# Optimization experiments

Measured on AMD Instinct MI355X. Metric: run time of the kernel, lower is better.

Reference implementation:

```python
import jax, jax.numpy as jnp
import numpy as np
import math

N, D, H, KV, DH, E, F_, CH = 2048, 1024, 16, 4, 64, 8, 2048, 64
VOCAB = 32000
EPS = 1e-6
THETA = 10000.0
DT = 0.1
BASE_SCALE = 10.0


def rmsnorm(x, w):
    var = jnp.mean(jnp.square(x), axis=-1, keepdims=True)
    return x * jax.lax.rsqrt(var + EPS) * w


def rope_tables(positions):
    inv_freq = THETA ** (-jnp.arange(0, DH, 2, dtype=jnp.float32) / DH)  # [DH/2]
    ang = positions.astype(jnp.float32)[:, None] * inv_freq              # [N, DH/2]
    return jnp.cos(ang), jnp.sin(ang)


def apply_rotary(x, cos, sin):
    # x: [N, heads, DH]; NeoX half-split rotation
    x1, x2 = jnp.split(x, 2, axis=-1)
    c, s = cos[:, None, :], sin[:, None, :]
    return jnp.concatenate([x1 * c - x2 * s, x2 * c + x1 * s], axis=-1)


def setup_inputs() -> dict:
    key = jax.random.key(0)
    ks = jax.random.split(key, 20)
    nrm = lambda k, shp, std: (jax.random.normal(k, shp) * std).astype(jnp.float32)
    inp = {
        'hidden': jax.random.normal(ks[0], (N, D), jnp.float32),
        'positions': jnp.arange(N, dtype=jnp.int32),
        'velocity': jax.random.normal(ks[1], (N, D), jnp.float32) * 0.1,
        'token_ids': jax.random.randint(ks[2], (N,), 0, VOCAB),
        'mu_prev': jax.random.normal(ks[3], (N, D), jnp.float32) * 0.1,
        'ln1_w': jnp.ones((D,), jnp.float32),
        'ln2_w': jnp.ones((D,), jnp.float32),
        'wq': nrm(ks[4], (D, H * DH), 0.02),
        'wk': nrm(ks[5], (D, KV * DH), 0.02),
        'wv': nrm(ks[6], (D, KV * DH), 0.02),
        'wo': nrm(ks[7], (H * DH, D), 0.02),
        'w_mu_q': nrm(ks[8], (D, H * DH), 0.01),
        'w_mu_k': nrm(ks[9], (D, KV * DH), 0.01),
        'w_mu_v': nrm(ks[10], (D, KV * DH), 0.01),
        'qnorm_w': jnp.ones((DH,), jnp.float32),
        'knorm_w': jnp.ones((DH,), jnp.float32),
        'dyn_mu': jnp.zeros((D,), jnp.float32),
        'dyn_mu_proj_w': nrm(ks[11], (D, D), 0.01),
        'ctrl_in_w': nrm(ks[12], (2 * D, CH), 0.02),
        'ctrl_in_b': jnp.zeros((CH,), jnp.float32),
        'ctrl_out_w': nrm(ks[13], (CH, 3 * D), 0.01),
        'ctrl_out_b': jnp.concatenate([jnp.full((D,), 2.2), jnp.full((D,), -2.2), jnp.zeros((D,))]).astype(jnp.float32),
        'mu_router_w': nrm(ks[14], (D, E), 0.01),
        'w_gate': nrm(ks[15], (E, D, F_), 0.02),
        'w_up': nrm(ks[16], (E, D, F_), 0.02),
        'w_down': nrm(ks[17], (E, F_, D), 0.02),
    }
    return inp


def reference(hidden, positions, velocity, token_ids, mu_prev,
              ln1_w, ln2_w, wq, wk, wv, wo, w_mu_q, w_mu_k, w_mu_v,
              qnorm_w, knorm_w, dyn_mu, dyn_mu_proj_w,
              ctrl_in_w, ctrl_in_b, ctrl_out_w, ctrl_out_b,
              mu_router_w, w_gate, w_up, w_down):
    residual = hidden
    h = rmsnorm(hidden, ln1_w)
    # --- mu-guided GQA attention ---
    q = (h @ wq + mu_prev @ w_mu_q).reshape(N, H, DH)
    k = (h @ wk + mu_prev @ w_mu_k).reshape(N, KV, DH)
    v = (h @ wv + mu_prev @ w_mu_v).reshape(N, KV, DH)
    q = rmsnorm(q, qnorm_w)
    k = rmsnorm(k, knorm_w)
    cos, sin = rope_tables(positions)
    q = apply_rotary(q, cos, sin)
    k = apply_rotary(k, cos, sin)
    groups = H // KV
    k = jnp.repeat(k, groups, axis=1)  # [N, H, DH]
    v = jnp.repeat(v, groups, axis=1)
    scale = 1.0 / math.sqrt(DH)
    scores = jnp.einsum('nhd,mhd->hnm', q, k) * scale
    attn = jax.nn.softmax(scores, axis=-1)
    o = jnp.einsum('hnm,mhd->nhd', attn, v).reshape(N, H * DH) @ wo
    # --- INL dynamics (PID) ---
    hv = jnp.concatenate([o, velocity], axis=-1)
    ctrl = jax.nn.silu(hv @ ctrl_in_w + ctrl_in_b)
    co = ctrl @ ctrl_out_w + ctrl_out_b
    alpha_raw, beta_raw, gate_raw = co[:, :D], co[:, D:2 * D], co[:, 2 * D:]
    alpha = jax.nn.sigmoid(alpha_raw)
    beta = jnp.minimum(jax.nn.softplus(beta_raw), 2.0)
    gate = jax.nn.sigmoid(gate_raw)
    mu_cur = dyn_mu + o @ dyn_mu_proj_w
    err = o - mu_cur
    v_next = jnp.clip(alpha * velocity - beta * err, -10.0, 10.0)
    h_next = o + DT * gate * v_next
    hidden = residual + h_next
    # --- mu-guided token-routed MoE MLP ---
    residual2 = hidden
    x = rmsnorm(hidden, ln2_w)
    base_ids = (token_ids % E).astype(jnp.int32)
    mu_logits = mu_cur @ mu_router_w                        # [N, E]
    combined = jax.nn.one_hot(base_ids, E) * BASE_SCALE + mu_logits
    expert_ids = jnp.argmax(combined, axis=-1)              # [N]
    g = jnp.einsum('nd,edf->enf', x, w_gate)                # [E, N, F]
    u = jnp.einsum('nd,edf->enf', x, w_up)
    mid = jax.nn.silu(g) * u
    y_all = jnp.einsum('enf,efd->end', mid, w_down)         # [E, N, D]
    sel = jax.nn.one_hot(expert_ids, E)                     # [N, E]
    y = jnp.einsum('ne,end->nd', sel, y_all)
    hidden = residual2 + y
    return (hidden, v_next, mu_cur)
```

## Files before the change

### kernel.cpp

```cpp
#include <hip/hip_runtime.h>
#include <hip/hip_bf16.h>
#include <math.h>

typedef __hip_bfloat16 bf16;
typedef __attribute__((ext_vector_type(8))) short short8;
typedef __attribute__((ext_vector_type(4))) short short4v;
typedef __attribute__((ext_vector_type(4))) float floatx4;

#define N_TOK 2048
#define DM    1024
#define NH    16
#define NKV   4
#define DH    64
#define NE    8
#define FF    2048
#define CH    64
#define QSCL  0.18033688011112042f

__device__ __forceinline__ float b2f(bf16 x) { return __bfloat162float(x); }
__device__ __forceinline__ bf16  f2b(float x) { return __float2bfloat16(x); }
__device__ __forceinline__ short f2s(float x) { bf16 t = __float2bfloat16(x); return *(short*)&t; }

#define MFMA16(a, b, c) __builtin_amdgcn_mfma_f32_16x16x32_bf16(a, b, c, 0, 0, 0)

#define GLL16(g, l) __builtin_amdgcn_global_load_lds( \
    (const __attribute__((address_space(1))) void*)(g), \
    (__attribute__((address_space(3))) void*)(l), 16, 0, 0)

__device__ __forceinline__ float blockReduceSum256(float v) {
    __shared__ float tmp[4];
    #pragma unroll
    for (int m = 1; m < 64; m <<= 1) v += __shfl_xor(v, m, 64);
    if ((threadIdx.x & 63) == 0) tmp[threadIdx.x >> 6] = v;
    __syncthreads();
    float r = tmp[0] + tmp[1] + tmp[2] + tmp[3];
    __syncthreads();
    return r;
}

struct TEnt {
    const float* src; bf16* dst;
    long sstride, dstride;
    int sN, ldk, tN, tilesPer, start;
};
struct TTab { TEnt t[13]; };

template <int TK>
__global__ __launch_bounds__(256) void k_transpose_all(TTab tab, int base,
                                                       int* counts, int* fill) {
    if (base == 0 && blockIdx.x == 0 && threadIdx.x < NE) {
        counts[threadIdx.x] = 0;
        fill[threadIdx.x] = 0;
    }
    int b = blockIdx.x + base;
    int wi = 0;
    #pragma unroll
    for (int i = 1; i < 13; i++) if (b >= tab.t[i].start) wi = i;
    const TEnt& w = tab.t[wi];
    int local = b - w.start;
    int e = local / w.tilesPer; local -= e * w.tilesPer;
    int kt = local / w.tN, nt = local - kt * w.tN;
    const float* s = w.src + (long)e * w.sstride + (long)(kt * TK) * w.sN + nt * 64;
    bf16* d = w.dst + (long)e * w.dstride + (long)(nt * 64) * w.ldk + kt * TK;

    __shared__ short t16[64 * TK];
    int tid = threadIdx.x;
    int c4 = (tid & 15) * 4;

    #pragma unroll
    for (int j = 0; j < (TK / 8 + 15) / 16; j++) {
        int kk8 = 8 * ((tid >> 4) + 16 * j);
        if (kk8 < TK) {
            float4 rr[8];
            #pragma unroll
            for (int t = 0; t < 8; t++)
                rr[t] = *(const float4*)(s + (long)(kk8 + t) * w.sN + c4);
            #pragma unroll
            for (int q = 0; q < 4; q++) {
                int n = c4 + q;
                int ks = kk8 ^ ((n & 7) << 3);
                short8 o;
                #pragma unroll
                for (int t = 0; t < 8; t++) o[t] = f2s(((const float*)&rr[t])[q]);
                *(short8*)&t16[n * TK + ks] = o;
            }
        }
    }
    __syncthreads();
    const int cpr = TK / 8;
    #pragma unroll
    for (int rnd = 0; rnd < TK / 32; rnd++) {
        int id = tid + rnd * 256;
        int n = id / cpr;
        int kc = (id % cpr) * 8;
        int ks = kc ^ ((n & 7) << 3);
        short8 o = *(const short8*)&t16[n * TK + ks];
        *(short8*)(d + (long)n * w.ldk + kc) = o;
    }
}

__global__ __launch_bounds__(256) void k_prep(
    const float* __restrict__ hidden, const float* __restrict__ ln1_w,
    const float* __restrict__ mu_prev, const float* __restrict__ velocity,
    bf16* __restrict__ catA, bf16* __restrict__ ctrlA)
{
    int n = blockIdx.x, tid = threadIdx.x;
    float ss = 0.f, vals[4];
    #pragma unroll
    for (int i = 0; i < 4; i++) {
        int c = tid + i * 256;
        vals[i] = hidden[(long)n * DM + c];
        ss += vals[i] * vals[i];
        catA[(long)n * 2048 + 1024 + c] = f2b(mu_prev[(long)n * DM + c]);
        ctrlA[(long)n * 2048 + 1024 + c] = f2b(velocity[(long)n * DM + c]);
    }
    float tot = blockReduceSum256(ss);
    float r = rsqrtf(tot / (float)DM + 1e-6f);
    #pragma unroll
    for (int i = 0; i < 4; i++) {
        int c = tid + i * 256;
        catA[(long)n * 2048 + c] = f2b(vals[i] * r * ln1_w[c]);
    }
}

#define GEMM_WRITE  1
#define GEMM_BIAS   2
#define GEMM_WRITEB 4
#define GEMM_DOWN   8

__global__ __launch_bounds__(256) void k_gemm(
    const bf16* __restrict__ A, int lda,
    const bf16* __restrict__ Bt, int ldb, long strideBe,
    float* __restrict__ C, int ldc,
    const float* __restrict__ bias,
    bf16* __restrict__ Cb, int ldcb,
    int K, int flags,
    int nsplit, long strideKc,
    const int* __restrict__ grp_cnt,
    const int* __restrict__ perm,
    float* __restrict__ outp)
{
    __shared__ __align__(16) short As[128 * 32];
    __shared__ __align__(16) short Bs[128 * 32];
    int tid = threadIdx.x;
    int e = blockIdx.z, kc = 0;
    if (nsplit > 1) { e = blockIdx.z / nsplit; kc = blockIdx.z % nsplit; }
    int rowBase, rowsValid;
    const bf16* Bp = Bt;
    if (grp_cnt) {
        int r0 = 0;
        #pragma unroll
        for (int i = 0; i < NE; i++) r0 += (i < e) ? grp_cnt[i] : 0;
        int r1 = r0 + grp_cnt[e];
        int rt = blockIdx.y * 128;
        rowsValid = (r1 - r0) - rt;
        if (rowsValid <= 0) return;
        if (rowsValid > 128) rowsValid = 128;
        rowBase = r0 + rt;
        Bp = Bt + (long)e * strideBe;
    } else {
        rowBase = blockIdx.y * 128;
        rowsValid = 128;
    }
    int n0 = blockIdx.x * 128;
    int Kc = K / nsplit;
    int kbeg = kc * Kc, kend = kbeg + Kc;

    floatx4 acc[4][4];
    #pragma unroll
    for (int i = 0; i < 4; i++)
        #pragma unroll
        for (int j = 0; j < 4; j++) acc[i][j] = (floatx4){0.f, 0.f, 0.f, 0.f};

    int wave = tid >> 6, lane = tid & 63;
    int wm = (wave >> 1) * 64, wn = (wave & 1) * 64;
    int lrow = lane & 15, quad = lane >> 4;

    int c0 = wave * 2;
    int srow0 = c0 * 16 + (lane >> 2);
    int srow1 = (c0 + 1) * 16 + (lane >> 2);
    int skoff = (lane & 3) * 8;
    short* ldsA0 = As + c0 * 512;
    short* ldsA1 = As + (c0 + 1) * 512;
    short* ldsB0 = Bs + c0 * 512;
    short* ldsB1 = Bs + (c0 + 1) * 512;

    for (int k0 = kbeg; k0 < kend; k0 += 32) {
        if (srow0 < rowsValid) GLL16(A + (long)(rowBase + srow0) * lda + k0 + skoff, ldsA0);
        if (srow1 < rowsValid) GLL16(A + (long)(rowBase + srow1) * lda + k0 + skoff, ldsA1);
        GLL16(Bp + (long)(n0 + srow0) * ldb + k0 + skoff, ldsB0);
        GLL16(Bp + (long)(n0 + srow1) * ldb + k0 + skoff, ldsB1);
        __syncthreads();
        short8 af[4], bfr[4];
        #pragma unroll
        for (int mi = 0; mi < 4; mi++)
            af[mi] = *(const short8*)(&As[(wm + mi * 16 + lrow) * 32 + quad * 8]);
        #pragma unroll
        for (int ni = 0; ni < 4; ni++)
            bfr[ni] = *(const short8*)(&Bs[(wn + ni * 16 + lrow) * 32 + quad * 8]);
        #pragma unroll
        for (int mi = 0; mi < 4; mi++)
            #pragma unroll
            for (int ni = 0; ni < 4; ni++)
                acc[mi][ni] = MFMA16(af[mi], bfr[ni], acc[mi][ni]);
        __syncthreads();
    }

    #pragma unroll
    for (int mi = 0; mi < 4; mi++) {
        #pragma unroll
        for (int ni = 0; ni < 4; ni++) {
            #pragma unroll
            for (int r = 0; r < 4; r++) {
                int rl = wm + mi * 16 + quad * 4 + r;
                if (rl >= rowsValid) continue;
                int grow = rowBase + rl;
                int gcol = n0 + wn + ni * 16 + lrow;
                float v = acc[mi][ni][r];
                if (nsplit > 1) {
                    C[kc * strideKc + (long)grow * ldc + gcol] = v;
                    continue;
                }
                if (flags & GEMM_BIAS) v += bias[gcol];
                if (flags & GEMM_DOWN) {
                    int tok = perm[grow];
                    float* o = &outp[(long)tok * ldc + gcol];
                    *o = *o + v;
                } else {
                    if (flags & GEMM_WRITE) C[(long)grow * ldc + gcol] = v;
                    if (flags & GEMM_WRITEB) Cb[(long)grow * ldcb + gcol] = f2b(v);
                }
            }
        }
    }
}

__global__ __launch_bounds__(256) void k_red_wo(const float* __restrict__ p,
                                                float* __restrict__ o_f,
                                                bf16* __restrict__ ctrlA) {
    int n = blockIdx.x, tid = threadIdx.x;
    #pragma unroll
    for (int i = 0; i < 4; i++) {
        int c = tid + i * 256;
        float v = p[(long)n * DM + c] + p[(long)N_TOK * DM + (long)n * DM + c];
        o_f[(long)n * DM + c] = v;
        ctrlA[(long)n * 2048 + c] = f2b(v);
    }
}

__global__ __launch_bounds__(256) void k_red_down(const float* __restrict__ p,
                                                  const int* __restrict__ perm,
                                                  float* __restrict__ out0) {
    int r = blockIdx.x, tid = threadIdx.x;
    int tok = perm[r];
    #pragma unroll
    for (int i = 0; i < 4; i++) {
        int c = tid + i * 256;
        long idx = (long)r * DM + c;
        float v = p[idx] + p[(long)N_TOK * DM + idx] +
                  p[(long)2 * N_TOK * DM + idx] + p[(long)3 * N_TOK * DM + idx];
        out0[(long)tok * DM + c] += v;
    }
}

__global__ __launch_bounds__(256) void k_ctrl_gemm(
    const bf16* __restrict__ A,
    const bf16* __restrict__ Bt,
    float* __restrict__ part)
{
    __shared__ __align__(16) short As[128 * 32];
    __shared__ __align__(16) short Bs[64 * 32];
    int tid = threadIdx.x;
    int rowBase = blockIdx.x * 128;
    int kbeg = blockIdx.y * 256;
    int wave = tid >> 6, lane = tid & 63;
    int wm = wave * 32, lrow = lane & 15, quad = lane >> 4;
    int srow = lane >> 2, skoff = (lane & 3) * 8;

    floatx4 acc[2][4];
    #pragma unroll
    for (int i = 0; i < 2; i++)
        #pragma unroll
        for (int j = 0; j < 4; j++) acc[i][j] = (floatx4){0.f, 0.f, 0.f, 0.f};

    short* ldsA0 = As + (wave * 2) * 512;
    short* ldsA1 = As + (wave * 2 + 1) * 512;
    short* ldsB  = Bs + wave * 512;

    for (int k0 = kbeg; k0 < kbeg + 256; k0 += 32) {
        GLL16(A + (long)(rowBase + wave * 32 + srow) * 2048 + k0 + skoff, ldsA0);
        GLL16(A + (long)(rowBase + wave * 32 + 16 + srow) * 2048 + k0 + skoff, ldsA1);
        GLL16(Bt + (long)(wave * 16 + srow) * 2048 + k0 + skoff, ldsB);
        __syncthreads();
        short8 af[2], bfr[4];
        af[0] = *(const short8*)(&As[(wm + lrow) * 32 + quad * 8]);
        af[1] = *(const short8*)(&As[(wm + 16 + lrow) * 32 + quad * 8]);
        #pragma unroll
        for (int ni = 0; ni < 4; ni++)
            bfr[ni] = *(const short8*)(&Bs[(ni * 16 + lrow) * 32 + quad * 8]);
        #pragma unroll
        for (int mi = 0; mi < 2; mi++)
            #pragma unroll
            for (int ni = 0; ni < 4; ni++)
                acc[mi][ni] = MFMA16(af[mi], bfr[ni], acc[mi][ni]);
        __syncthreads();
    }
    #pragma unroll
    for (int mi = 0; mi < 2; mi++)
        #pragma unroll
        for (int ni = 0; ni < 4; ni++)
            #pragma unroll
            for (int r = 0; r < 4; r++) {
                int grow = rowBase + wm + mi * 16 + quad * 4 + r;
                part[((long)blockIdx.y * N_TOK + grow) * 64 + ni * 16 + lrow] = acc[mi][ni][r];
            }
}

__global__ __launch_bounds__(256) void k_silu_ctrl(const float* __restrict__ part,
                                                   const float* __restrict__ b,
                                                   bf16* __restrict__ out) {
    int i4 = (blockIdx.x * 256 + threadIdx.x) * 4;
    float4 a = *(const float4*)(b + (i4 & 63));
    #pragma unroll
    for (int kc = 0; kc < 8; kc++) {
        float4 p = *(const float4*)(part + (long)kc * (N_TOK * 64) + i4);
        a.x += p.x; a.y += p.y; a.z += p.z; a.w += p.w;
    }
    short4v o;
    o[0] = f2s(a.x / (1.f + __expf(-a.x)));
    o[1] = f2s(a.y / (1.f + __expf(-a.y)));
    o[2] = f2s(a.z / (1.f + __expf(-a.z)));
    o[3] = f2s(a.w / (1.f + __expf(-a.w)));
    *(short4v*)(out + i4) = o;
}

__global__ __launch_bounds__(256) void k_qkv_post(
    const float* __restrict__ qkvp, const int* __restrict__ positions,
    const float* __restrict__ qnw, const float* __restrict__ knw,
    bf16* __restrict__ q, bf16* __restrict__ k, bf16* __restrict__ v)
{
    int n = blockIdx.x;
    int wave = threadIdx.x >> 6, lane = threadIdx.x & 63;
    float pos = (float)positions[n];
    int i = lane & 31;
    float invf = exp2f(-(float)(2 * i) * (13.287712379549449f / 64.f));
    float ang = pos * invf;
    float c = cosf(ang), s = sinf(ang);

    #pragma unroll
    for (int si = 0; si < 6; si++) {
        int slot = wave + si * 4;
        long base = (long)n * 1536 +
                    (slot < 16 ? slot * 64
                               : (slot < 20 ? 1024 + (slot - 16) * 64
                                            : 1280 + (slot - 20) * 64));
        float val = qkvp[base + lane] + qkvp[(long)N_TOK * 1536 + base + lane];
        if (slot < 20) {
            float ss = val * val;
            #pragma unroll
            for (int m = 1; m < 64; m <<= 1) ss += __shfl_xor(ss, m, 64);
            float r = rsqrtf(ss / 64.f + 1e-6f);
            float wn = (slot < 16 ? qnw[lane] : knw[lane]);
            float xn = val * r * wn;
            float partner = __shfl_xor(xn, 32, 64);
            float out = (lane < 32) ? (xn * c - partner * s) : (xn * c + partner * s);
            if (slot < 16) q[((long)n * NH + slot) * 64 + lane] = f2b(out * QSCL);
            else           k[((long)n * NKV + (slot - 16)) * 64 + lane] = f2b(out);
        } else {
            v[((long)n * NKV + (slot - 20)) * 64 + lane] = f2b(val);
        }
    }
}

__global__ __launch_bounds__(256) void k_vt(const bf16* __restrict__ v,
                                            bf16* __restrict__ vt) {
    __shared__ short tile[64][65];
    int kv = blockIdx.z, n0 = blockIdx.x * 64;
    int tid = threadIdx.x;
    int c = tid & 63, r4 = tid >> 6;
    const short* vs = (const short*)v;
    #pragma unroll
    for (int i = 0; i < 16; i++) {
        int r = i * 4 + r4;
        tile[r][c] = vs[(long)(n0 + r) * 256 + kv * 64 + c];
    }
    __syncthreads();
    #pragma unroll
    for (int i = 0; i < 16; i++) {
        int d = i * 4 + r4;
        ((short*)vt)[(long)(kv * 64 + d) * 2048 + n0 + c] = tile[c][d];
    }
}

__device__ __forceinline__ int lds_idx(int row, int col_sh) {
    int byteoff = col_sh * 2;
    byteoff ^= (row & 7) << 4;
    return row * 64 + (byteoff >> 1);
}

__global__ __launch_bounds__(256) void k_attn(
    const bf16* __restrict__ q, const bf16* __restrict__ k,
    const bf16* __restrict__ vt,
    float* __restrict__ opart, float2* __restrict__ ml)
{
    const int h = blockIdx.y;
    const int qbase = blockIdx.x * 64;
    const int z = blockIdx.z;
    const int kvh = h >> 2;
    __shared__ __align__(16) short Ks[64 * 64];
    __shared__ __align__(16) short Vt[64 * 64];
    __shared__ __align__(16) short Ps[64 * 64];
    int tid = threadIdx.x, wave = tid >> 6, lane = tid & 63;
    int lrow = lane & 15, quad = lane >> 4;

    const bf16* qp = q + ((long)(qbase + wave * 16 + lrow) * NH + h) * 64;
    short8 aq0 = *(const short8*)(qp + quad * 8);
    short8 aq1 = *(const short8*)(qp + 32 + quad * 8);

    short8 bones;
    #pragma unroll
    for (int j = 0; j < 8; j++) bones[j] = (short)0x3F80;

    const int lin0 = tid, lin1 = tid + 256;
    const int sr0 = lin0 >> 3, sc0 = (lin0 & 7) * 8;
    const int sr1 = lin1 >> 3, sc1 = (lin1 & 7) * 8;
    const int wi0 = lds_idx(sr0, sc0), wi1 = lds_idx(sr1, sc1);

    const int kt0 = z * (N_TOK / 4);
    const bf16* kg0 = k + ((long)(kt0 + sr0) * NKV + kvh) * 64 + sc0;
    const bf16* kg1 = k + ((long)(kt0 + sr1) * NKV + kvh) * 64 + sc1;
    const bf16* vg0 = vt + (long)(kvh * 64 + sr0) * 2048 + kt0 + sc0;
    const bf16* vg1 = vt + (long)(kvh * 64 + sr1) * 2048 + kt0 + sc1;

    *(short8*)&Ks[wi0] = *(const short8*)kg0;
    *(short8*)&Ks[wi1] = *(const short8*)kg1;
    *(short8*)&Vt[wi0] = *(const short8*)vg0;
    *(short8*)&Vt[wi1] = *(const short8*)vg1;

    float m_i[4];
    floatx4 lacc = (floatx4){0.f, 0.f, 0.f, 0.f};
    floatx4 oacc[4];
    #pragma unroll
    for (int r = 0; r < 4; r++) m_i[r] = -1e30f;
    #pragma unroll
    for (int di = 0; di < 4; di++) oacc[di] = (floatx4){0.f, 0.f, 0.f, 0.f};
    __syncthreads();

    const int NT = (N_TOK / 4) / 64;
    for (int t = 0; t < NT; t++) {
        bool pf = (t + 1 < NT);
        short8 nk0, nk1, nv0, nv1;
        if (pf) {
            long ko = (long)(t + 1) * (64 * NKV * 64);
            int  vo = (t + 1) * 64;
            nk0 = *(const short8*)(kg0 + ko);
            nk1 = *(const short8*)(kg1 + ko);
            nv0 = *(const short8*)(vg0 + vo);
            nv1 = *(const short8*)(vg1 + vo);
        }

        floatx4 sv[4];
        __builtin_amdgcn_s_setprio(1);
        #pragma unroll
        for (int kn = 0; kn < 4; kn++) {
            short8 b0 = *(const short8*)&Ks[lds_idx(kn * 16 + lrow, quad * 8)];
            short8 b1 = *(const short8*)&Ks[lds_idx(kn * 16 + lrow, 32 + quad * 8)];
            floatx4 tt = (floatx4){0.f, 0.f, 0.f, 0.f};
            tt = MFMA16(aq0, b0, tt);
            tt = MFMA16(aq1, b1, tt);
            sv[kn] = tt;
        }
        __builtin_amdgcn_s_setprio(0);

        float mx[4];
        #pragma unroll
        for (int r = 0; r < 4; r++) {
            float m0 = fmaxf(fmaxf(sv[0][r], sv[1][r]), fmaxf(sv[2][r], sv[3][r]));
            #pragma unroll
            for (int msk = 1; msk < 16; msk <<= 1) m0 = fmaxf(m0, __shfl_xor(m0, msk, 64));
            mx[r] = m0;
        }
        int ok = (mx[0] <= m_i[0] + 8.f) & (mx[1] <= m_i[1] + 8.f) &
                 (mx[2] <= m_i[2] + 8.f) & (mx[3] <= m_i[3] + 8.f);
        if (!__all(ok)) {
            #pragma unroll
            for (int r = 0; r < 4; r++) {
                float mn = fmaxf(m_i[r], mx[r]);
                float al = exp2f(m_i[r] - mn);
                m_i[r] = mn;
                lacc[r] *= al;
                #pragma unroll
                for (int di = 0; di < 4; di++) oacc[di][r] *= al;
            }
        }
        #pragma unroll
        for (int kn = 0; kn < 4; kn++)
            #pragma unroll
            for (int r = 0; r < 4; r++)
                sv[kn][r] = exp2f(sv[kn][r] - m_i[r]);

        #pragma unroll
        for (int kn = 0; kn < 4; kn++)
            #pragma unroll
            for (int r = 0; r < 4; r++)
                Ps[lds_idx(wave * 16 + quad * 4 + r, kn * 16 + lrow)] = f2s(sv[kn][r]);
        __syncthreads();

        short8 ap0 = *(const short8*)&Ps[lds_idx(wave * 16 + lrow, quad * 8)];
        short8 ap1 = *(const short8*)&Ps[lds_idx(wave * 16 + lrow, 32 + quad * 8)];
        __builtin_amdgcn_s_setprio(1);
        lacc = MFMA16(ap0, bones, lacc);
        lacc = MFMA16(ap1, bones, lacc);
        #pragma unroll
        for (int di = 0; di < 4; di++) {
            short8 bv0 = *(const short8*)&Vt[lds_idx(di * 16 + lrow, quad * 8)];
            short8 bv1 = *(const short8*)&Vt[lds_idx(di * 16 + lrow, 32 + quad * 8)];
            oacc[di] = MFMA16(ap0, bv0, oacc[di]);
            oacc[di] = MFMA16(ap1, bv1, oacc[di]);
        }
        __builtin_amdgcn_s_setprio(0);
        __syncthreads();

        if (pf) {
            *(short8*)&Ks[wi0] = nk0;
            *(short8*)&Ks[wi1] = nk1;
            *(short8*)&Vt[wi0] = nv0;
            *(short8*)&Vt[wi1] = nv1;
            __syncthreads();
        }
    }

    #pragma unroll
    for (int di = 0; di < 4; di++)
        #pragma unroll
        for (int r = 0; r < 4; r++) {
            int n = qbase + wave * 16 + quad * 4 + r;
            opart[((long)z * N_TOK + n) * DM + h * 64 + di * 16 + lrow] = oacc[di][r];
        }
    if (lrow == 0) {
        #pragma unroll
        for (int r = 0; r < 4; r++) {
            int n = qbase + wave * 16 + quad * 4 + r;
            ml[(long)(z * NH + h) * N_TOK + n] = make_float2(m_i[r], lacc[r]);
        }
    }
}

__global__ __launch_bounds__(256) void k_attn_merge(
    const float* __restrict__ opart, const float2* __restrict__ ml,
    bf16* __restrict__ attn_out)
{
    int n = blockIdx.x, tid = threadIdx.x;
    __shared__ float2 sml[4][NH];
    if (tid < 64) {
        int zz = tid >> 4, hh = tid & 15;
        sml[zz][hh] = ml[(long)(zz * NH + hh) * N_TOK + n];
    }
    __syncthreads();
    #pragma unroll
    for (int i = 0; i < 4; i++) {
        int c = tid + i * 256;
        int h = c >> 6;
        float M = fmaxf(fmaxf(sml[0][h].x, sml[1][h].x),
                        fmaxf(sml[2][h].x, sml[3][h].x));
        float num = 0.f, den = 0.f;
        #pragma unroll
        for (int zz = 0; zz < 4; zz++) {
            float w = exp2f(sml[zz][h].x - M);
            num += w * opart[((long)zz * N_TOK + n) * DM + c];
            den += w * sml[zz][h].y;
        }
        attn_out[(long)n * DM + c] = f2b(num / den);
    }
}

__global__ __launch_bounds__(256) void k_ode(
    const float* __restrict__ co, const float* __restrict__ o_f,
    const float* __restrict__ velocity, const float* __restrict__ mup,
    const float* __restrict__ dyn_mu, const float* __restrict__ hidden_in,
    const float* __restrict__ mu_router_w, const int* __restrict__ token_ids,
    const float* __restrict__ ln2_w,
    float* __restrict__ out0, float* __restrict__ out_vnext,
    float* __restrict__ out_mu, bf16* __restrict__ x_bf,
    int* __restrict__ expert_id, int* __restrict__ counts)
{
    int n = blockIdx.x, tid = threadIdx.x;
    __shared__ float mu_s[DM];
    __shared__ float red2[32][8];

    #pragma unroll
    for (int i = 0; i < 4; i++) {
        int c = tid + i * 256;
        mu_s[c] = mup[(long)n * DM + c] + mup[(long)N_TOK * DM + (long)n * DM + c]
                + dyn_mu[c];
    }
    __syncthreads();

    {
        int e = tid & 7, kc = tid >> 3;
        float a = 0.f;
        #pragma unroll
        for (int kk = 0; kk < 32; kk++) {
            int k = kc * 32 + kk;
            a += mu_s[k] * mu_router_w[k * NE + e];
        }
        red2[kc][e] = a;
    }
    __syncthreads();
    if (tid == 0) {
        int bid = token_ids[n] & (NE - 1);
        float best = -1e30f; int bi = 0;
        for (int e = 0; e < NE; e++) {
            float lg = (e == bid ? 10.f : 0.f);
            for (int j = 0; j < 32; j++) lg += red2[j][e];
            if (lg > best) { best = lg; bi = e; }
        }
        expert_id[n] = bi;
        atomicAdd(&counts[bi], 1);
    }

    float ssq = 0.f;
    float h1v[4];
    #pragma unroll
    for (int i = 0; i < 4; i++) {
        int c = tid + i * 256;
        float coa = co[(long)n * 3072 + c];
        float cob = co[(long)n * 3072 + DM + c];
        float cog = co[(long)n * 3072 + 2 * DM + c];
        float alpha = 1.f / (1.f + __expf(-coa));
        float sp = (cob > 20.f) ? cob : log1pf(__expf(cob));
        float beta = fminf(sp, 2.0f);
        float gate = 1.f / (1.f + __expf(-cog));
        float ov = o_f[(long)n * DM + c];
        float vv = velocity[(long)n * DM + c];
        float err = ov - mu_s[c];
        float vn = fminf(fmaxf(alpha * vv - beta * err, -10.f), 10.f);
        float hn = ov + 0.1f * gate * vn;
        float h1 = hidden_in[(long)n * DM + c] + hn;
        h1v[i] = h1;
        ssq += h1 * h1;
        out_vnext[(long)n * DM + c] = vn;
        out_mu[(long)n * DM + c] = mu_s[c];
        out0[(long)n * DM + c] = h1;
    }
    float tot = blockReduceSum256(ssq);
    float rstd = rsqrtf(tot / (float)DM + 1e-6f);
    #pragma unroll
    for (int i = 0; i < 4; i++) {
        int c = tid + i * 256;
        x_bf[(long)n * DM + c] = f2b(h1v[i] * rstd * ln2_w[c]);
    }
}

__global__ __launch_bounds__(256) void k_scatter_gather(
    const int* __restrict__ expert_id, const int* __restrict__ counts,
    int* __restrict__ fill, int* __restrict__ perm,
    const bf16* __restrict__ x, bf16* __restrict__ xg)
{
    int n = blockIdx.x * 4 + (threadIdx.x >> 6);
    int lane = threadIdx.x & 63;
    int e = expert_id[n];
    int p = 0;
    if (lane == 0) {
        int off = 0;
        #pragma unroll
        for (int i = 0; i < NE; i++) off += (i < e) ? counts[i] : 0;
        p = off + atomicAdd(&fill[e], 1);
        perm[p] = n;
    }
    p = __shfl(p, 0, 64);
    const int4* s = (const int4*)(x + (long)n * DM);
    int4* d = (int4*)(xg + (long)p * DM);
    d[lane] = s[lane];
    d[lane + 64] = s[lane + 64];
}

__global__ __launch_bounds__(256) void k_silumul(const bf16* __restrict__ gu,
                                                 bf16* __restrict__ mid) {
    long i = ((long)blockIdx.x * 256 + threadIdx.x) * 8;
    long r = i >> 11, c = i & 2047;
    short8 g8 = *(const short8*)(gu + r * 4096 + c);
    short8 u8 = *(const short8*)(gu + r * 4096 + 2048 + c);
    short8 o;
    #pragma unroll
    for (int j = 0; j < 8; j++) {
        short gs = g8[j], us = u8[j];
        float g = b2f(*(bf16*)&gs);
        float u = b2f(*(bf16*)&us);
        o[j] = f2s(g / (1.f + __expf(-g)) * u);
    }
    *(short8*)(mid + i) = o;
}

extern "C" void kernel_launch(void* const* d_in, const int* in_sizes, int n_in,
                              void* d_out, int out_size, void* d_ws, size_t ws_size,
                              hipStream_t stream) {
    (void)in_sizes; (void)n_in; (void)out_size; (void)ws_size;
    const float* hidden     = (const float*)d_in[0];
    const int*   positions  = (const int*)d_in[1];
    const float* velocity   = (const float*)d_in[2];
    const int*   token_ids  = (const int*)d_in[3];
    const float* mu_prev    = (const float*)d_in[4];
    const float* ln1_w      = (const float*)d_in[5];
    const float* ln2_w      = (const float*)d_in[6];
    const float* wq         = (const float*)d_in[7];
    const float* wk         = (const float*)d_in[8];
    const float* wv         = (const float*)d_in[9];
    const float* wo         = (const float*)d_in[10];
    const float* w_mu_q     = (const float*)d_in[11];
    const float* w_mu_k     = (const float*)d_in[12];
    const float* w_mu_v     = (const float*)d_in[13];
    const float* qnorm_w    = (const float*)d_in[14];
    const float* knorm_w    = (const float*)d_in[15];
    const float* dyn_mu     = (const float*)d_in[16];
    const float* dyn_proj   = (const float*)d_in[17];
    const float* ctrl_in_w  = (const float*)d_in[18];
    const float* ctrl_in_b  = (const float*)d_in[19];
    const float* ctrl_out_w = (const float*)d_in[20];
    const float* ctrl_out_b = (const float*)d_in[21];
    const float* mu_router  = (const float*)d_in[22];
    const float* w_gate     = (const float*)d_in[23];
    const float* w_up       = (const float*)d_in[24];
    const float* w_down     = (const float*)d_in[25];

    float* out0 = (float*)d_out;
    float* out1 = out0 + (long)N_TOK * DM;
    float* out2 = out1 + (long)N_TOK * DM;

    char* p = (char*)d_ws;
    auto alloc = [&](size_t bytes) -> void* {
        void* r = (void*)p;
        p += (bytes + 255) & ~(size_t)255;
        return r;
    };
    bf16* WqkvT   = (bf16*)alloc((long)1536 * 2048 * 2);
    bf16* woT     = (bf16*)alloc((long)1024 * 1024 * 2);
    bf16* dynT    = (bf16*)alloc((long)1024 * 1024 * 2);
    bf16* ctrlinT = (bf16*)alloc((long)64 * 2048 * 2);
    bf16* ctrloutT= (bf16*)alloc((long)3072 * 64 * 2);
    bf16* gupT    = (bf16*)alloc((long)NE * 4096 * 1024 * 2);
    bf16* downT   = (bf16*)alloc((long)NE * 1024 * 2048 * 2);
    bf16*  catA   = (bf16*)alloc((long)N_TOK * 2048 * 2);
    bf16*  ctrlA  = (bf16*)alloc((long)N_TOK * 2048 * 2);
    float* xbuf   = (float*)alloc((long)N_TOK * 1536 * 4);
    bf16*  q_bf   = (bf16*)alloc((long)N_TOK * NH * DH * 2);
    bf16*  k_bf   = (bf16*)alloc((long)N_TOK * NKV * DH * 2);
    bf16*  v_bf   = (bf16*)alloc((long)N_TOK * NKV * DH * 2);
    bf16*  vt_bf  = (bf16*)alloc((long)NKV * DH * N_TOK * 2);
    float* o_f    = (float*)alloc((long)N_TOK * DM * 4);
    float* coGu   = (float*)alloc((long)N_TOK * 3072 * 4);
    float* splitb = (float*)alloc((long)4 * N_TOK * DM * 4);
    bf16*  ctrlbf = (bf16*)alloc((long)N_TOK * CH * 2);
    int*   expert_id = (int*)alloc(N_TOK * 4);
    int*   perm      = (int*)alloc(N_TOK * 4);
    int*   counts    = (int*)alloc(64 * 4);
    int*   fill      = (int*)alloc(64 * 4);

    bf16*  attn_bf = catA;
    bf16*  x_bf    = (bf16*)xbuf;
    bf16*  xg_bf   = (bf16*)xbuf + (long)N_TOK * DM;
    float* cpart   = (float*)((bf16*)xbuf + (long)2 * N_TOK * DM);
    float* opart   = splitb;
    float2* ml     = (float2*)coGu;
    float* co_f    = coGu;
    bf16*  gu_bf   = (bf16*)coGu;
    bf16*  mid_bf  = (bf16*)o_f;

    dim3 blk(256);

    TTab tt; int st = 0;
    auto ent = [&](int i, const float* s, bf16* d, long ss, long ds,
                   int sN, int ldk, int tN, int tK, int nE) {
        tt.t[i].src = s; tt.t[i].dst = d;
        tt.t[i].sstride = ss; tt.t[i].dstride = ds;
        tt.t[i].sN = sN; tt.t[i].ldk = ldk;
        tt.t[i].tN = tN; tt.t[i].tilesPer = tN * tK;
        tt.t[i].start = st;
        st += tN * tK * nE;
    };
    ent(0,  wq,         WqkvT,                          0, 0, 1024, 2048, 16, 4, 1);
    ent(1,  wk,         WqkvT + (long)1024 * 2048,      0, 0, 256,  2048,  4, 4, 1);
    ent(2,  wv,         WqkvT + (long)1280 * 2048,      0, 0, 256,  2048,  4, 4, 1);
    ent(3,  w_mu_q,     WqkvT + 1024,                   0, 0, 1024, 2048, 16, 4, 1);
    ent(4,  w_mu_k,     WqkvT + (long)1024 * 2048 + 1024, 0, 0, 256, 2048, 4, 4, 1);
    ent(5,  w_mu_v,     WqkvT + (long)1280 * 2048 + 1024, 0, 0, 256, 2048, 4, 4, 1);
    ent(6,  wo,         woT,                            0, 0, 1024, 1024, 16, 4, 1);
    ent(7,  dyn_proj,   dynT,                           0, 0, 1024, 1024, 16, 4, 1);
    ent(8,  ctrl_in_w,  ctrlinT,                        0, 0, 64,   2048,  1, 8, 1);
    ent(9,  w_gate,     gupT,                  (long)1024 * 2048, (long)4096 * 1024, 2048, 1024, 32, 4, 8);
    ent(10, w_up,       gupT + (long)2048 * 1024, (long)1024 * 2048, (long)4096 * 1024, 2048, 1024, 32, 4, 8);
    ent(11, w_down,     downT,                 (long)2048 * 1024, (long)1024 * 2048, 1024, 2048, 16, 8, 8);
    int stMain = st;
    ent(12, ctrl_out_w, ctrloutT,                       0, 0, 3072, 64,   48, 1, 1);
    k_transpose_all<256><<<stMain, blk, 0, stream>>>(tt, 0, counts, fill);
    k_transpose_all<64><<<st - stMain, blk, 0, stream>>>(tt, stMain, counts, fill);

    k_prep<<<N_TOK, blk, 0, stream>>>(hidden, ln1_w, mu_prev, velocity, catA, ctrlA);

    k_gemm<<<dim3(12,16,2), blk, 0, stream>>>(catA, 2048, WqkvT, 2048, 0,
        splitb, 1536, nullptr, nullptr, 0, 2048, 0, 2, (long)N_TOK * 1536,
        nullptr, nullptr, nullptr);

    k_qkv_post<<<N_TOK, blk, 0, stream>>>(splitb, positions, qnorm_w, knorm_w, q_bf, k_bf, v_bf);
    k_vt<<<dim3(32,1,NKV), blk, 0, stream>>>(v_bf, vt_bf);
    k_attn<<<dim3(32,16,4), blk, 0, stream>>>(q_bf, k_bf, vt_bf, opart, ml);
    k_attn_merge<<<N_TOK, blk, 0, stream>>>(opart, ml, attn_bf);

    k_gemm<<<dim3(8,16,2), blk, 0, stream>>>(attn_bf, 1024, woT, 1024, 0,
        splitb, 1024, nullptr, nullptr, 0, 1024, 0, 2, (long)N_TOK * DM,
        nullptr, nullptr, nullptr);
    k_red_wo<<<N_TOK, blk, 0, stream>>>(splitb, o_f, ctrlA);

    k_gemm<<<dim3(8,16,2), blk, 0, stream>>>(ctrlA, 2048, dynT, 1024, 0,
        splitb, 1024, nullptr, nullptr, 0, 1024, 0, 2, (long)N_TOK * DM,
        nullptr, nullptr, nullptr);

    k_ctrl_gemm<<<dim3(16,8,1), blk, 0, stream>>>(ctrlA, ctrlinT, cpart);
    k_silu_ctrl<<<(N_TOK * CH) / 1024, blk, 0, stream>>>(cpart, ctrl_in_b, ctrlbf);
    k_gemm<<<dim3(24,16,1), blk, 0, stream>>>(ctrlbf, 64, ctrloutT, 64, 0,
        co_f, 3072, ctrl_out_b, nullptr, 0, 64, GEMM_WRITE | GEMM_BIAS, 1, 0,
        nullptr, nullptr, nullptr);

    k_ode<<<N_TOK, blk, 0, stream>>>(co_f, o_f, velocity, splitb, dyn_mu, hidden,
        mu_router, token_ids, ln2_w, out0, out1, out2, x_bf, expert_id, counts);

    k_scatter_gather<<<N_TOK / 4, blk, 0, stream>>>(expert_id, counts, fill, perm,
        x_bf, xg_bf);

    k_gemm<<<dim3(32,16,NE), blk, 0, stream>>>(xg_bf, 1024, gupT, 1024, (long)4096*1024,
        nullptr, 0, nullptr, gu_bf, 4096, 1024, GEMM_WRITEB, 1, 0,
        counts, nullptr, nullptr);
    k_silumul<<<(N_TOK * FF) / (256 * 8), blk, 0, stream>>>(gu_bf, mid_bf);
    k_gemm<<<dim3(8,16,NE*4), blk, 0, stream>>>(mid_bf, 2048, downT, 2048, (long)1024*2048,
        splitb, 1024, nullptr, nullptr, 0, 2048, 0, 4, (long)N_TOK * DM,
        counts, nullptr, nullptr);
    k_red_down<<<N_TOK, blk, 0, stream>>>(splitb, perm, out0);
}
```

Before: 634.5 us.

## Read fp32 MoE expert weights directly in grouped GEMM, skip bf16 pre-transpose

The separate transpose/convert pass that turned the fp32 gate/up/down expert weights into bf16 transposed copies is removed. A new GEMM kernel loads fp32 weight tiles straight into LDS, converts them to bf16 and transposes them in shared memory before the MFMA loop. This avoids writing and re-reading large bf16 weight copies (about 200MB of fp32 weights in total). The cost is twice the global B-tile bytes per block, since every row tile re-reads the fp32 weights, plus an extra LDS conversion step and sync.

```diff
diff --git a/kernel.cpp b/kernel.cpp
--- a/kernel.cpp
+++ b/kernel.cpp
@@ -126,7 +126,6 @@
 #define GEMM_WRITE  1
 #define GEMM_BIAS   2
 #define GEMM_WRITEB 4
-#define GEMM_DOWN   8
 
 __global__ __launch_bounds__(256) void k_gemm(
     const bf16* __restrict__ A, int lda,
@@ -136,9 +135,7 @@
     bf16* __restrict__ Cb, int ldcb,
     int K, int flags,
     int nsplit, long strideKc,
-    const int* __restrict__ grp_cnt,
-    const int* __restrict__ perm,
-    float* __restrict__ outp)
+    const int* __restrict__ grp_cnt)
 {
     __shared__ __align__(16) short As[128 * 32];
     __shared__ __align__(16) short Bs[128 * 32];
@@ -222,13 +219,123 @@
                     continue;
                 }
                 if (flags & GEMM_BIAS) v += bias[gcol];
-                if (flags & GEMM_DOWN) {
-                    int tok = perm[grow];
-                    float* o = &outp[(long)tok * ldc + gcol];
-                    *o = *o + v;
-                } else {
-                    if (flags & GEMM_WRITE) C[(long)grow * ldc + gcol] = v;
-                    if (flags & GEMM_WRITEB) Cb[(long)grow * ldcb + gcol] = f2b(v);
+                if (flags & GEMM_WRITE) C[(long)grow * ldc + gcol] = v;
+                if (flags & GEMM_WRITEB) Cb[(long)grow * ldcb + gcol] = f2b(v);
+            }
+        }
+    }
+}
+
+__global__ __launch_bounds__(256) void k_gemm_f32b(
+    const bf16* __restrict__ A, int lda,
+    const float* __restrict__ Bf0, const float* __restrict__ Bf1,
+    int ldbn, long strideBfe, int nbf0,
+    float* __restrict__ C, int ldc,
+    bf16* __restrict__ Cb, int ldcb,
+    int K, int flags,
+    int nsplit, long strideKc,
+    const int* __restrict__ grp_cnt)
+{
+    __shared__ __align__(16) short As[128 * 32];
+    __shared__ __align__(16) float Braw[32 * 128];
+    __shared__ __align__(16) short Bs2[128 * 40];
+    int tid = threadIdx.x;
+    int e = blockIdx.z, kc = 0;
+    if (nsplit > 1) { e = blockIdx.z / nsplit; kc = blockIdx.z % nsplit; }
+    int r0 = 0;
+    #pragma unroll
+    for (int i = 0; i < NE; i++) r0 += (i < e) ? grp_cnt[i] : 0;
+    int r1 = r0 + grp_cnt[e];
+    int rt = blockIdx.y * 128;
+    int rowsValid = (r1 - r0) - rt;
+    if (rowsValid <= 0) return;
+    if (rowsValid > 128) rowsValid = 128;
+    int rowBase = r0 + rt;
+
+    int n0 = blockIdx.x * 128;
+    const float* Bsrc;
+    int nb;
+    if (n0 < nbf0) { Bsrc = Bf0; nb = n0; }
+    else           { Bsrc = Bf1; nb = n0 - nbf0; }
+    Bsrc += (long)e * strideBfe;
+
+    int Kc = K / nsplit;
+    int kbeg = kc * Kc, kend = kbeg + Kc;
+
+    floatx4 acc[4][4];
+    #pragma unroll
+    for (int i = 0; i < 4; i++)
+        #pragma unroll
+        for (int j = 0; j < 4; j++) acc[i][j] = (floatx4){0.f, 0.f, 0.f, 0.f};
+
+    int wave = tid >> 6, lane = tid & 63;
+    int wm = (wave >> 1) * 64, wn = (wave & 1) * 64;
+    int lrow = lane & 15, quad = lane >> 4;
+
+    int c0 = wave * 2;
+    int srow0 = c0 * 16 + (lane >> 2);
+    int srow1 = (c0 + 1) * 16 + (lane >> 2);
+    int skoff = (lane & 3) * 8;
+    short* ldsA0 = As + c0 * 512;
+    short* ldsA1 = As + (c0 + 1) * 512;
+
+    int kB = wave * 2 + (lane >> 5);
+    int ncB = (lane & 31) * 4;
+
+    for (int k0 = kbeg; k0 < kend; k0 += 32) {
+        if (srow0 < rowsValid) GLL16(A + (long)(rowBase + srow0) * lda + k0 + skoff, ldsA0);
+        if (srow1 < rowsValid) GLL16(A + (long)(rowBase + srow1) * lda + k0 + skoff, ldsA1);
+        #pragma unroll
+        for (int r = 0; r < 4; r++)
+            GLL16(Bsrc + (long)(k0 + r * 8 + kB) * ldbn + nb + ncB,
+                  Braw + r * 1024 + wave * 256);
+        __syncthreads();
+
+        #pragma unroll
+        for (int r2 = 0; r2 < 4; r2++) {
+            int id = r2 * 256 + tid;
+            int n = id & 127, kb = id >> 7;
+            float f0 = Braw[(kb * 4 + 0) * 128 + n];
+            float f1 = Braw[(kb * 4 + 1) * 128 + n];
+            float f2 = Braw[(kb * 4 + 2) * 128 + n];
+            float f3 = Braw[(kb * 4 + 3) * 128 + n];
+            short4v o;
+            o[0] = f2s(f0); o[1] = f2s(f1); o[2] = f2s(f2); o[3] = f2s(f3);
+            *(short4v*)&Bs2[n * 40 + kb * 4] = o;
+        }
+        short8 af[4];
+        #pragma unroll
+        for (int mi = 0; mi < 4; mi++)
+            af[mi] = *(const short8*)(&As[(wm + mi * 16 + lrow) * 32 + quad * 8]);
+        __syncthreads();
+
+        short8 bfr[4];
+        #pragma unroll
+        for (int ni = 0; ni < 4; ni++)
+            bfr[ni] = *(const short8*)(&Bs2[(wn + ni * 16 + lrow) * 40 + quad * 8]);
+        #pragma unroll
+        for (int mi = 0; mi < 4; mi++)
+            #pragma unroll
+            for (int ni = 0; ni < 4; ni++)
+                acc[mi][ni] = MFMA16(af[mi], bfr[ni], acc[mi][ni]);
+    }
+    __syncthreads();
+
+    #pragma unroll
+    for (int mi = 0; mi < 4; mi++) {
+        #pragma unroll
+        for (int ni = 0; ni < 4; ni++) {
+            #pragma unroll
+            for (int r = 0; r < 4; r++) {
+                int rl = wm + mi * 16 + quad * 4 + r;
+                if (rl >= rowsValid) continue;
+                int grow = rowBase + rl;
+                int gcol = n0 + wn + ni * 16 + lrow;
+                float v = acc[mi][ni][r];
+                if (nsplit > 1) {
+                    C[kc * strideKc + (long)grow * ldc + gcol] = v;
+                } else if (flags & GEMM_WRITEB) {
+                    Cb[(long)grow * ldcb + gcol] = f2b(v);
                 }
             }
         }
@@ -738,8 +845,6 @@
     bf16* dynT    = (bf16*)alloc((long)1024 * 1024 * 2);
     bf16* ctrlinT = (bf16*)alloc((long)64 * 2048 * 2);
     bf16* ctrloutT= (bf16*)alloc((long)3072 * 64 * 2);
-    bf16* gupT    = (bf16*)alloc((long)NE * 4096 * 1024 * 2);
-    bf16* downT   = (bf16*)alloc((long)NE * 1024 * 2048 * 2);
     bf16*  catA   = (bf16*)alloc((long)N_TOK * 2048 * 2);
     bf16*  ctrlA  = (bf16*)alloc((long)N_TOK * 2048 * 2);
     float* xbuf   = (float*)alloc((long)N_TOK * 1536 * 4);
@@ -768,7 +873,8 @@
 
     dim3 blk(256);
 
-    TTab tt; int st = 0;
+    TTab tt{};
+    int st = 0;
     auto ent = [&](int i, const float* s, bf16* d, long ss, long ds,
                    int sN, int ldk, int tN, int tK, int nE) {
         tt.t[i].src = s; tt.t[i].dst = d;
@@ -787,11 +893,11 @@
     ent(6,  wo,         woT,                            0, 0, 1024, 1024, 16, 4, 1);
     ent(7,  dyn_proj,   dynT,                           0, 0, 1024, 1024, 16, 4, 1);
     ent(8,  ctrl_in_w,  ctrlinT,                        0, 0, 64,   2048,  1, 8, 1);
-    ent(9,  w_gate,     gupT,                  (long)1024 * 2048, (long)4096 * 1024, 2048, 1024, 32, 4, 8);
-    ent(10, w_up,       gupT + (long)2048 * 1024, (long)1024 * 2048, (long)4096 * 1024, 2048, 1024, 32, 4, 8);
-    ent(11, w_down,     downT,                 (long)2048 * 1024, (long)1024 * 2048, 1024, 2048, 16, 8, 8);
     int stMain = st;
-    ent(12, ctrl_out_w, ctrloutT,                       0, 0, 3072, 64,   48, 1, 1);
+    ent(9,  ctrl_out_w, ctrloutT,                       0, 0, 3072, 64,   48, 1, 1);
+    tt.t[10].start = 0x7fffffff;
+    tt.t[11].start = 0x7fffffff;
+    tt.t[12].start = 0x7fffffff;
     k_transpose_all<256><<<stMain, blk, 0, stream>>>(tt, 0, counts, fill);
     k_transpose_all<64><<<st - stMain, blk, 0, stream>>>(tt, stMain, counts, fill);
 
@@ -799,7 +905,7 @@
 
     k_gemm<<<dim3(12,16,2), blk, 0, stream>>>(catA, 2048, WqkvT, 2048, 0,
         splitb, 1536, nullptr, nullptr, 0, 2048, 0, 2, (long)N_TOK * 1536,
-        nullptr, nullptr, nullptr);
+        nullptr);
 
     k_qkv_post<<<N_TOK, blk, 0, stream>>>(splitb, positions, qnorm_w, knorm_w, q_bf, k_bf, v_bf);
     k_vt<<<dim3(32,1,NKV), blk, 0, stream>>>(v_bf, vt_bf);
@@ -808,18 +914,18 @@
 
     k_gemm<<<dim3(8,16,2), blk, 0, stream>>>(attn_bf, 1024, woT, 1024, 0,
         splitb, 1024, nullptr, nullptr, 0, 1024, 0, 2, (long)N_TOK * DM,
-        nullptr, nullptr, nullptr);
+        nullptr);
     k_red_wo<<<N_TOK, blk, 0, stream>>>(splitb, o_f, ctrlA);
 
     k_gemm<<<dim3(8,16,2), blk, 0, stream>>>(ctrlA, 2048, dynT, 1024, 0,
         splitb, 1024, nullptr, nullptr, 0, 1024, 0, 2, (long)N_TOK * DM,
-        nullptr, nullptr, nullptr);
+        nullptr);
 
     k_ctrl_gemm<<<dim3(16,8,1), blk, 0, stream>>>(ctrlA, ctrlinT, cpart);
     k_silu_ctrl<<<(N_TOK * CH) / 1024, blk, 0, stream>>>(cpart, ctrl_in_b, ctrlbf);
     k_gemm<<<dim3(24,16,1), blk, 0, stream>>>(ctrlbf, 64, ctrloutT, 64, 0,
         co_f, 3072, ctrl_out_b, nullptr, 0, 64, GEMM_WRITE | GEMM_BIAS, 1, 0,
-        nullptr, nullptr, nullptr);
+        nullptr);
 
     k_ode<<<N_TOK, blk, 0, stream>>>(co_f, o_f, velocity, splitb, dyn_mu, hidden,
         mu_router, token_ids, ln2_w, out0, out1, out2, x_bf, expert_id, counts);
@@ -827,12 +933,12 @@
     k_scatter_gather<<<N_TOK / 4, blk, 0, stream>>>(expert_id, counts, fill, perm,
         x_bf, xg_bf);
 
-    k_gemm<<<dim3(32,16,NE), blk, 0, stream>>>(xg_bf, 1024, gupT, 1024, (long)4096*1024,
-        nullptr, 0, nullptr, gu_bf, 4096, 1024, GEMM_WRITEB, 1, 0,
-        counts, nullptr, nullptr);
+    k_gemm_f32b<<<dim3(32,16,NE), blk, 0, stream>>>(xg_bf, 1024,
+        w_gate, w_up, 2048, (long)1024 * 2048, 2048,
+        nullptr, 0, gu_bf, 4096, 1024, GEMM_WRITEB, 1, 0, counts);
     k_silumul<<<(N_TOK * FF) / (256 * 8), blk, 0, stream>>>(gu_bf, mid_bf);
-    k_gemm<<<dim3(8,16,NE*4), blk, 0, stream>>>(mid_bf, 2048, downT, 2048, (long)1024*2048,
-        splitb, 1024, nullptr, nullptr, 0, 2048, 0, 4, (long)N_TOK * DM,
-        counts, nullptr, nullptr);
+    k_gemm_f32b<<<dim3(8,16,NE*4), blk, 0, stream>>>(mid_bf, 2048,
+        w_down, w_down, 1024, (long)2048 * 1024, 1 << 30,
+        splitb, 1024, nullptr, 0, 2048, 0, 4, (long)N_TOK * DM, counts);
     k_red_down<<<N_TOK, blk, 0, stream>>>(splitb, perm, out0);
 }
```

Result: faster. 578.1 us (-8.9%).
